# Kernel tuning notes

Measured on AMD Instinct MI355X. Metric: run time of the kernel, lower is better.

## Reference

```python
import jax, jax.numpy as jnp
import numpy as np

N_EMBD = 1024
HEAD_SIZE = 64
B, T = 4, 4096


def setup_inputs() -> dict:
    key = jax.random.key(0)
    kx, kk, kq, kv = jax.random.split(key, 4)
    s = 1.0 / np.sqrt(N_EMBD)
    return {
        "x": jax.random.normal(kx, (B, T, N_EMBD), dtype=jnp.float32),
        "Wk": jax.random.normal(kk, (N_EMBD, HEAD_SIZE), dtype=jnp.float32) * s,
        "Wq": jax.random.normal(kq, (N_EMBD, HEAD_SIZE), dtype=jnp.float32) * s,
        "Wv": jax.random.normal(kv, (N_EMBD, HEAD_SIZE), dtype=jnp.float32) * s,
    }


def reference(x, Wk, Wq, Wv):
    Bb, Tt, C = x.shape
    k = x @ Wk  # [B,T,H]
    q = x @ Wq
    v = x @ Wv
    # scores scaled by C**-0.5 where C = n_embd (as in the original module)
    w = jnp.einsum('bth,bsh->bts', q, k) * (C ** -0.5)  # [B,T,T]
    causal = jnp.tril(jnp.ones((Tt, Tt), dtype=bool))
    w = jnp.where(causal, w, -jnp.inf)
    w = jax.nn.softmax(w, axis=-1)
    # dropout prob is 0.0 (eval) -> identity
    out = jnp.einsum('bts,bsh->bth', w, v)  # [B,T,H]
    return out
```

## Files before the change

### kernel.cpp

```cpp
#include <hip/hip_runtime.h>


#define BSZ 4
#define TSZ 4096
#define CSZ 1024
#define MSZ (BSZ * TSZ)
#define QT 128
#define NQT (TSZ / QT)
#define CPB 272
#define MAXC 16

typedef _Float16 half8 __attribute__((ext_vector_type(8)));
typedef _Float16 half4 __attribute__((ext_vector_type(4)));
typedef float f32x4 __attribute__((ext_vector_type(4)));
typedef float f32x16 __attribute__((ext_vector_type(16)));

#define MFMA(a, b, c) __builtin_amdgcn_mfma_f32_16x16x32_f16((a), (b), (c), 0, 0, 0)
#define MFMA32(a, b, c) __builtin_amdgcn_mfma_f32_32x32x16_f16((a), (b), (c), 0, 0, 0)
#define QSCALE 0.04508422002778011f

__device__ __forceinline__ int kimg(int r, int h) {
    return r * 64 + (((h >> 3) ^ (r & 7)) << 3) + (h & 7);
}
__device__ __forceinline__ int vimg(int kk, int h) {
    return h * 64 + (((kk >> 3) ^ (h & 7)) << 3) + (kk & 7);
}

__device__ __forceinline__ void glds16(const _Float16* g, _Float16* l) {
    __builtin_amdgcn_global_load_lds(
        (const __attribute__((address_space(1))) void*)g,
        (__attribute__((address_space(3))) void*)l, 16, 0, 0);
}

__global__ __launch_bounds__(192) void wconv(const float* __restrict__ Wk,
                                             const float* __restrict__ Wq,
                                             const float* __restrict__ Wv,
                                             _Float16* __restrict__ Wt) {
    int k = blockIdx.x;
    int n = threadIdx.x;
    int g = k >> 6, c = (k >> 3) & 7, j = k & 7;
    const float* W = (n < 64) ? Wk : ((n < 128) ? Wq : Wv);
    float v = W[k * 64 + (n & 63)];
    if (n >= 64 && n < 128) v *= QSCALE;
    Wt[(size_t)n * 1024 + g * 64 + ((c ^ (n & 7)) << 3) + j] = (_Float16)v;
}

__global__ __launch_bounds__(512) void qkv_proj(
    const float* __restrict__ x, const _Float16* __restrict__ Wt,
    _Float16* __restrict__ qbf, _Float16* __restrict__ kvs) {
    __shared__ _Float16 wt[2][192 * 64];
    __shared__ _Float16 xt[2][64 * 64];

    int tid = threadIdx.x;
    int wave = tid >> 6, lane = tid & 63;
    int quad = lane >> 4, l16 = lane & 15;
    int id = blockIdx.x;
    int xcd = id & 7;
    int rb = (id >> 3) * 2 + (xcd & 1);
    int row0 = (xcd >> 1) * TSZ + rb * 64;
    int mh = wave >> 2;
    int ctb = (wave & 3) * 3;

    f32x4 acc[6];
#pragma unroll
    for (int i = 0; i < 6; i++) acc[i] = (f32x4){0.f, 0.f, 0.f, 0.f};

    int sr = tid >> 3, sc = tid & 7;
    const float* xrow = x + (size_t)(row0 + sr) * CSZ + sc * 8;
    f32x4 p0 = *(const f32x4*)xrow;
    f32x4 p1 = *(const f32x4*)(xrow + 4);

#pragma unroll
    for (int i = 0; i < 3; i++) {
        int g = i * 512 + tid;
        glds16(Wt + ((size_t)(g >> 3)) * 1024 + (g & 7) * 8,
               &wt[0][(size_t)g * 8]);
    }

    int cur = 0;
    for (int kc = 0; kc < CSZ; kc += 64, cur ^= 1) {
        {
            _Float16 tmp[8] __attribute__((aligned(16)));
#pragma unroll
            for (int i = 0; i < 4; i++) {
                tmp[i] = (_Float16)p0[i];
                tmp[4 + i] = (_Float16)p1[i];
            }
            *(half8*)&xt[cur][sr * 64 + ((sc ^ (sr & 7)) << 3)] = *(half8*)tmp;
        }
        __syncthreads();

        if (kc + 64 < CSZ) {
#pragma unroll
            for (int i = 0; i < 3; i++) {
                int g = i * 512 + tid;
                glds16(Wt + ((size_t)(g >> 3)) * 1024 + (kc + 64) + (g & 7) * 8,
                       &wt[cur ^ 1][(size_t)g * 8]);
            }
            p0 = *(const f32x4*)(xrow + kc + 64);
            p1 = *(const f32x4*)(xrow + kc + 68);
        }

#pragma unroll
        for (int ss = 0; ss < 2; ss++) {
            half8 a0 = *(half8*)&xt[cur][(mh * 32 + l16) * 64 +
                                         (((ss * 4 + quad) ^ (l16 & 7)) << 3)];
            half8 a1 = *(half8*)&xt[cur][(mh * 32 + 16 + l16) * 64 +
                                         (((ss * 4 + quad) ^ (l16 & 7)) << 3)];
#pragma unroll
            for (int j = 0; j < 3; j++) {
                int ct = ctb + j;
                half8 bb = *(half8*)&wt[cur][(ct * 16 + l16) * 64 +
                                             (((ss * 4 + quad) ^ (l16 & 7))
                                              << 3)];
                acc[j * 2 + 0] = MFMA(a0, bb, acc[j * 2 + 0]);
                acc[j * 2 + 1] = MFMA(a1, bb, acc[j * 2 + 1]);
            }
        }
    }

#pragma unroll
    for (int j = 0; j < 3; j++) {
        int ct = ctb + j;
        int kind = ct >> 2;
        int col = (ct & 3) * 16 + l16;
#pragma unroll
        for (int m = 0; m < 2; m++) {
#pragma unroll
            for (int r = 0; r < 4; r++) {
                int row = row0 + mh * 32 + m * 16 + quad * 4 + r;
                _Float16 val = (_Float16)acc[j * 2 + m][r];
                if (kind == 0) {
                    kvs[((size_t)(row >> 6)) * 8192 + kimg(row & 63, col)] = val;
                } else if (kind == 1) {
                    qbf[(size_t)row * 64 + col] = val;
                } else {
                    kvs[((size_t)(row >> 6)) * 8192 + 4096 +
                        vimg(row & 63, col)] = val;
                }
            }
        }
    }
}

__global__ __launch_bounds__(256, 4) void attn_partial(
    const _Float16* __restrict__ qbf, const _Float16* __restrict__ kvs,
    _Float16* __restrict__ opart, float* __restrict__ ml) {
    __shared__ _Float16 kt[2][4096];
    __shared__ _Float16 vt[2][4096];
    __shared__ float ls[4][32];

    int tid = threadIdx.x;
    int wave = tid >> 6, lane = tid & 63;
    int l32 = lane & 31, hi = lane >> 5;

    int id = blockIdx.x;
    int xcd = id & 7;
    int b = xcd >> 1;
    int id2 = (id >> 3) * 2 + (xcd & 1);
    int qt = 0;
    while (qt < NQT - 1 && (((qt + 2) * (qt + 2)) >> 2) <= id2) qt++;
    int chunk = id2 - (((qt + 1) * (qt + 1)) >> 2);
    int nt = 2 * (qt + 1);
    int lo = chunk * 4;
    int hic = min(lo + 4, nt);
    int part = (b * NQT + qt) * MAXC + chunk;

    const _Float16* qb = qbf + (size_t)b * TSZ * 64;
    const _Float16* kvb = kvs + (size_t)b * 64 * 8192;

    int qrow = qt * QT + wave * 32 + l32;
    half8 aq[4];
#pragma unroll
    for (int ss = 0; ss < 4; ss++)
        aq[ss] = *(const half8*)&qb[(size_t)qrow * 64 + ss * 16 + hi * 8];

    f32x16 o[2];
#pragma unroll
    for (int i = 0; i < 16; i++) { o[0][i] = 0.f; o[1][i] = 0.f; }
    float l_acc = 0.f;

    int soff = wave * 512 + lane * 8;

    {
        const _Float16* p0 = kvb + (size_t)lo * 8192 + soff;
        glds16(p0, &kt[0][soff]);
        glds16(p0 + 2048, &kt[0][2048 + soff]);
        glds16(p0 + 4096, &vt[0][soff]);
        glds16(p0 + 6144, &vt[0][2048 + soff]);
    }

    int cur = 0;
    for (int kti = lo; kti < hic; kti++, cur ^= 1) {
        __syncthreads();
        if (kti + 1 < hic) {
            const _Float16* p0 = kvb + (size_t)(kti + 1) * 8192 + soff;
            glds16(p0, &kt[cur ^ 1][soff]);
            glds16(p0 + 2048, &kt[cur ^ 1][2048 + soff]);
            glds16(p0 + 4096, &vt[cur ^ 1][soff]);
            glds16(p0 + 6144, &vt[cur ^ 1][2048 + soff]);
        }

        bool diag = (kti >= 2 * qt);
        int qrel = qrow - kti * 64;
        int wmax = qt * QT + wave * 32 + 31 - kti * 64;

#pragma unroll
        for (int ctk = 0; ctk < 2; ctk++) {
            if (diag && ctk * 32 > wmax) continue;

            f32x16 s;
#pragma unroll
            for (int i = 0; i < 16; i++) s[i] = 0.f;
            __builtin_amdgcn_s_setprio(1);
#pragma unroll
            for (int ss = 0; ss < 4; ss++) {
                half8 ak = *(half8*)&kt[cur][kimg(ctk * 32 + l32,
                                                  ss * 16 + hi * 8)];
                s = MFMA32(ak, aq[ss], s);
            }
            __builtin_amdgcn_s_setprio(0);

            float e[16];
#pragma unroll
            for (int r = 0; r < 16; r++) {
                float ev = exp2f(s[r]);
                if (diag) {
                    int key = ctk * 32 + (r & 3) + 8 * (r >> 2) + 4 * hi;
                    if (key > qrel) ev = 0.f;
                }
                e[r] = ev;
                l_acc += ev;
            }

            unsigned pk[8];
#pragma unroll
            for (int p = 0; p < 8; p++) {
                auto h2 = __builtin_amdgcn_cvt_pkrtz(e[2 * p], e[2 * p + 1]);
                union { decltype(h2) h; unsigned u; } cv;
                cv.h = h2;
                pk[p] = cv.u;
            }
            asm("v_permlane32_swap_b32 %0, %1" : "+v"(pk[0]), "+v"(pk[2]));
            asm("v_permlane32_swap_b32 %0, %1" : "+v"(pk[1]), "+v"(pk[3]));
            asm("v_permlane32_swap_b32 %0, %1" : "+v"(pk[4]), "+v"(pk[6]));
            asm("v_permlane32_swap_b32 %0, %1" : "+v"(pk[5]), "+v"(pk[7]));
            union { unsigned u[4]; half8 h; } A0, A1;
            A0.u[0] = pk[0]; A0.u[1] = pk[1]; A0.u[2] = pk[2]; A0.u[3] = pk[3];
            A1.u[0] = pk[4]; A1.u[1] = pk[5]; A1.u[2] = pk[6]; A1.u[3] = pk[7];

            __builtin_amdgcn_s_setprio(1);
#pragma unroll
            for (int cth = 0; cth < 2; cth++) {
                int h = cth * 32 + l32;
                half8 v0 = *(half8*)&vt[cur][vimg((2 * ctk + 0) * 16 + hi * 8, h)];
                half8 v1 = *(half8*)&vt[cur][vimg((2 * ctk + 1) * 16 + hi * 8, h)];
                o[cth] = MFMA32(A0.h, v0, o[cth]);
                o[cth] = MFMA32(A1.h, v1, o[cth]);
            }
            __builtin_amdgcn_s_setprio(0);
        }
    }

    l_acc += __shfl_xor(l_acc, 32);
    float inv = l_acc > 0.f ? 1.f / l_acc : 0.f;
    if (!hi) ls[wave][l32] = inv;

    _Float16* op = opart + (size_t)part * (QT * 64);
#pragma unroll
    for (int r = 0; r < 16; r++) {
        int rl = (r & 3) + 8 * (r >> 2) + 4 * hi;
        float invr = ls[wave][rl];
        int lrow = wave * 32 + rl;
        op[lrow * 64 + l32] = (_Float16)(o[0][r] * invr);
        op[lrow * 64 + 32 + l32] = (_Float16)(o[1][r] * invr);
    }
    if (!hi) ml[part * QT + wave * 32 + l32] = l_acc;
}

__global__ __launch_bounds__(256) void combine(
    const _Float16* __restrict__ opart, const float* __restrict__ ml,
    float* __restrict__ out) {
    int tid = threadIdx.x;
    int id = blockIdx.x;
    int xcd = id & 7;
    int b = xcd >> 1;
    int rb = (id >> 3) * 2 + (xcd & 1);
    int row = b * TSZ + rb * 32 + (tid >> 3);
    int seg = (tid & 7) * 8;
    int qt = (row >> 7) & (NQT - 1);
    int prow = row & (QT - 1);
    int pbase = (b * NQT + qt) * MAXC;
    int nc = (qt + 2) >> 1;

    float acc[8];
#pragma unroll
    for (int i = 0; i < 8; i++) acc[i] = 0.f;
    float lsum = 0.f;
    for (int s = 0; s < nc; s++) {
        float l = ml[(pbase + s) * QT + prow];
        lsum += l;
        half8 h = *(const half8*)&opart[(size_t)(pbase + s) * (QT * 64) +
                                        prow * 64 + seg];
#pragma unroll
        for (int i = 0; i < 8; i++) acc[i] += l * (float)h[i];
    }
    float inv = 1.f / lsum;
    float* ob = out + (size_t)row * 64 + seg;
#pragma unroll
    for (int i = 0; i < 8; i++) ob[i] = acc[i] * inv;
}

extern "C" void kernel_launch(void* const* d_in, const int* in_sizes, int n_in,
                              void* d_out, int out_size, void* d_ws,
                              size_t ws_size, hipStream_t stream) {
    (void)in_sizes; (void)n_in; (void)out_size; (void)ws_size;
    const float* x = (const float*)d_in[0];
    const float* Wk = (const float*)d_in[1];
    const float* Wq = (const float*)d_in[2];
    const float* Wv = (const float*)d_in[3];

    _Float16* Wt = (_Float16*)d_ws;
    _Float16* qbf = Wt + 192 * 1024;
    _Float16* kvs = qbf + (size_t)MSZ * 64;
    _Float16* opart = kvs + (size_t)MSZ * 128;
    float* ml = (float*)(opart + (size_t)BSZ * NQT * MAXC * QT * 64);

    wconv<<<1024, 192, 0, stream>>>(Wk, Wq, Wv, Wt);
    qkv_proj<<<MSZ / 64, 512, 0, stream>>>(x, Wt, qbf, kvs);
    attn_partial<<<BSZ * CPB, 256, 0, stream>>>(qbf, kvs, opart, ml);
    combine<<<MSZ / 32, 256, 0, stream>>>(opart, ml, (float*)d_out);
}
```

Measured before the change: 144.1 us.

## Shrink projection tiles, drop setprio, use native exp2, write single-chunk rows directly

```diff
diff --git a/kernel.cpp b/kernel.cpp
--- a/kernel.cpp
+++ b/kernel.cpp
@@ -45,11 +45,11 @@
     Wt[(size_t)n * 1024 + g * 64 + ((c ^ (n & 7)) << 3) + j] = (_Float16)v;
 }
 
-__global__ __launch_bounds__(512) void qkv_proj(
+__global__ __launch_bounds__(256) void qkv_proj(
     const float* __restrict__ x, const _Float16* __restrict__ Wt,
     _Float16* __restrict__ qbf, _Float16* __restrict__ kvs) {
     __shared__ _Float16 wt[2][192 * 64];
-    __shared__ _Float16 xt[2][64 * 64];
+    __shared__ _Float16 xt[2][32 * 64];
 
     int tid = threadIdx.x;
     int wave = tid >> 6, lane = tid & 63;
@@ -57,9 +57,8 @@
     int id = blockIdx.x;
     int xcd = id & 7;
     int rb = (id >> 3) * 2 + (xcd & 1);
-    int row0 = (xcd >> 1) * TSZ + rb * 64;
-    int mh = wave >> 2;
-    int ctb = (wave & 3) * 3;
+    int row0 = (xcd >> 1) * TSZ + rb * 32;
+    int ctb = wave * 3;
 
     f32x4 acc[6];
 #pragma unroll
@@ -71,8 +70,8 @@
     f32x4 p1 = *(const f32x4*)(xrow + 4);
 
 #pragma unroll
-    for (int i = 0; i < 3; i++) {
-        int g = i * 512 + tid;
+    for (int i = 0; i < 6; i++) {
+        int g = i * 256 + tid;
         glds16(Wt + ((size_t)(g >> 3)) * 1024 + (g & 7) * 8,
                &wt[0][(size_t)g * 8]);
     }
@@ -92,8 +91,8 @@
 
         if (kc + 64 < CSZ) {
 #pragma unroll
-            for (int i = 0; i < 3; i++) {
-                int g = i * 512 + tid;
+            for (int i = 0; i < 6; i++) {
+                int g = i * 256 + tid;
                 glds16(Wt + ((size_t)(g >> 3)) * 1024 + (kc + 64) + (g & 7) * 8,
                        &wt[cur ^ 1][(size_t)g * 8]);
             }
@@ -103,9 +102,9 @@
 
 #pragma unroll
         for (int ss = 0; ss < 2; ss++) {
-            half8 a0 = *(half8*)&xt[cur][(mh * 32 + l16) * 64 +
+            half8 a0 = *(half8*)&xt[cur][l16 * 64 +
                                          (((ss * 4 + quad) ^ (l16 & 7)) << 3)];
-            half8 a1 = *(half8*)&xt[cur][(mh * 32 + 16 + l16) * 64 +
+            half8 a1 = *(half8*)&xt[cur][(16 + l16) * 64 +
                                          (((ss * 4 + quad) ^ (l16 & 7)) << 3)];
 #pragma unroll
             for (int j = 0; j < 3; j++) {
@@ -128,7 +127,7 @@
         for (int m = 0; m < 2; m++) {
 #pragma unroll
             for (int r = 0; r < 4; r++) {
-                int row = row0 + mh * 32 + m * 16 + quad * 4 + r;
+                int row = row0 + m * 16 + quad * 4 + r;
                 _Float16 val = (_Float16)acc[j * 2 + m][r];
                 if (kind == 0) {
                     kvs[((size_t)(row >> 6)) * 8192 + kimg(row & 63, col)] = val;
@@ -145,7 +144,8 @@
 
 __global__ __launch_bounds__(256, 4) void attn_partial(
     const _Float16* __restrict__ qbf, const _Float16* __restrict__ kvs,
-    _Float16* __restrict__ opart, float* __restrict__ ml) {
+    _Float16* __restrict__ opart, float* __restrict__ ml,
+    float* __restrict__ out) {
     __shared__ _Float16 kt[2][4096];
     __shared__ _Float16 vt[2][4096];
     __shared__ float ls[4][32];
@@ -164,6 +164,7 @@
     int nt = 2 * (qt + 1);
     int lo = chunk * 4;
     int hic = min(lo + 4, nt);
+    int nc = (qt + 2) >> 1;
     int part = (b * NQT + qt) * MAXC + chunk;
 
     const _Float16* qb = qbf + (size_t)b * TSZ * 64;
@@ -212,19 +213,17 @@
             f32x16 s;
 #pragma unroll
             for (int i = 0; i < 16; i++) s[i] = 0.f;
-            __builtin_amdgcn_s_setprio(1);
 #pragma unroll
             for (int ss = 0; ss < 4; ss++) {
                 half8 ak = *(half8*)&kt[cur][kimg(ctk * 32 + l32,
                                                   ss * 16 + hi * 8)];
                 s = MFMA32(ak, aq[ss], s);
             }
-            __builtin_amdgcn_s_setprio(0);
 
             float e[16];
 #pragma unroll
             for (int r = 0; r < 16; r++) {
-                float ev = exp2f(s[r]);
+                float ev = __builtin_amdgcn_exp2f(s[r]);
                 if (diag) {
                     int key = ctk * 32 + (r & 3) + 8 * (r >> 2) + 4 * hi;
                     if (key > qrel) ev = 0.f;
@@ -249,7 +248,6 @@
             A0.u[0] = pk[0]; A0.u[1] = pk[1]; A0.u[2] = pk[2]; A0.u[3] = pk[3];
             A1.u[0] = pk[4]; A1.u[1] = pk[5]; A1.u[2] = pk[6]; A1.u[3] = pk[7];
 
-            __builtin_amdgcn_s_setprio(1);
 #pragma unroll
             for (int cth = 0; cth < 2; cth++) {
                 int h = cth * 32 + l32;
@@ -258,13 +256,25 @@
                 o[cth] = MFMA32(A0.h, v0, o[cth]);
                 o[cth] = MFMA32(A1.h, v1, o[cth]);
             }
-            __builtin_amdgcn_s_setprio(0);
         }
     }
 
     l_acc += __shfl_xor(l_acc, 32);
     float inv = l_acc > 0.f ? 1.f / l_acc : 0.f;
     if (!hi) ls[wave][l32] = inv;
+
+    if (nc == 1) {
+        float* ob = out + ((size_t)(b * TSZ + qt * QT)) * 64;
+#pragma unroll
+        for (int r = 0; r < 16; r++) {
+            int rl = (r & 3) + 8 * (r >> 2) + 4 * hi;
+            float invr = ls[wave][rl];
+            int lrow = wave * 32 + rl;
+            ob[lrow * 64 + l32] = o[0][r] * invr;
+            ob[lrow * 64 + 32 + l32] = o[1][r] * invr;
+        }
+        return;
+    }
 
     _Float16* op = opart + (size_t)part * (QT * 64);
 #pragma unroll
@@ -289,9 +299,10 @@
     int row = b * TSZ + rb * 32 + (tid >> 3);
     int seg = (tid & 7) * 8;
     int qt = (row >> 7) & (NQT - 1);
+    int nc = (qt + 2) >> 1;
+    if (nc == 1) return;
     int prow = row & (QT - 1);
     int pbase = (b * NQT + qt) * MAXC;
-    int nc = (qt + 2) >> 1;
 
     float acc[8];
 #pragma unroll
@@ -327,7 +338,8 @@
     float* ml = (float*)(opart + (size_t)BSZ * NQT * MAXC * QT * 64);
 
     wconv<<<1024, 192, 0, stream>>>(Wk, Wq, Wv, Wt);
-    qkv_proj<<<MSZ / 64, 512, 0, stream>>>(x, Wt, qbf, kvs);
-    attn_partial<<<BSZ * CPB, 256, 0, stream>>>(qbf, kvs, opart, ml);
+    qkv_proj<<<MSZ / 32, 256, 0, stream>>>(x, Wt, qbf, kvs);
+    attn_partial<<<BSZ * CPB, 256, 0, stream>>>(qbf, kvs, opart, ml,
+                                                (float*)d_out);
     combine<<<MSZ / 32, 256, 0, stream>>>(opart, ml, (float*)d_out);
 }
```

Result: slower. 147.2 us (+2.1%).
